# Optimization experiments

Hardware: AMD Instinct MI355X
Metric: run time of the kernel (lower is better)

Reference implementation:

```python
import jax, jax.numpy as jnp
import numpy as np

B, L, S, D, H, NS, NSLOT = 2, 2048, 2048, 1024, 16, 8, 512
HD = D // H


def _silu(x):
    return x * jax.nn.sigmoid(x)


def _layernorm(x, g, b, eps=1e-5):
    mu = jnp.mean(x, axis=-1, keepdims=True)
    var = jnp.var(x, axis=-1, keepdims=True)
    return (x - mu) * jax.lax.rsqrt(var + eps) * g + b


def setup_inputs() -> dict:
    key = jax.random.key(0)
    ks = jax.random.split(key, 12)
    x_q = jax.random.normal(ks[0], (B, L, D), dtype=jnp.float32)
    x_idx = jax.random.randint(ks[1], (B, S), 0, NSLOT)
    E_slots = jax.random.normal(ks[2], (NSLOT, D), dtype=jnp.float32)
    # EMA decay rates close to 1 so multi-scale gates stay non-degenerate over S steps
    rhos = 1.0 - 0.005 * jax.random.uniform(ks[3], (NS,), dtype=jnp.float32)
    C_seq = jax.random.uniform(ks[4], (B, L, NS), dtype=jnp.float32)
    s = 1.0 / np.sqrt(D)
    Wq = jax.random.normal(ks[5], (D, D), dtype=jnp.float32) * s
    Wk = jax.random.normal(ks[6], (D, D), dtype=jnp.float32) * s
    Wv = jax.random.normal(ks[7], (D, D), dtype=jnp.float32) * s
    Wo = jax.random.normal(ks[8], (D, D), dtype=jnp.float32) * s
    Wpe = jax.random.normal(ks[9], (D, NS), dtype=jnp.float32) * (1.0 / np.sqrt(NS))
    ln_kv_g = jnp.ones((D,), jnp.float32); ln_kv_b = jnp.zeros((D,), jnp.float32)
    ln_q_g = jnp.ones((D,), jnp.float32); ln_q_b = jnp.zeros((D,), jnp.float32)
    return dict(x_q=x_q, x_idx=x_idx, E_slots=E_slots, rhos=rhos, C_seq=C_seq,
                Wq=Wq, Wk=Wk, Wv=Wv, Wo=Wo, Wpe=Wpe,
                ln_kv_g=ln_kv_g, ln_kv_b=ln_kv_b, ln_q_g=ln_q_g, ln_q_b=ln_q_b)


def reference(x_q, x_idx, E_slots, rhos, C_seq, Wq, Wk, Wv, Wo, Wpe,
              ln_kv_g, ln_kv_b, ln_q_g, ln_q_b):
    # --- KV side: memory = ln_kv(E_slots); K/V = proj(memory); gather by slot id ---
    mem = _layernorm(E_slots, ln_kv_g, ln_kv_b)          # [NSLOT, D]
    Ek = mem @ Wk.T                                       # [NSLOT, D]
    Ev = mem @ Wv.T
    K = Ek[x_idx]                                         # [B, S, D] embedding lookup
    V = Ev[x_idx]
    # --- multiplicative EMA gate per kv position: c[s,m] = rho_m^(age) ---
    ages = (S - 1 - jnp.arange(S)).astype(x_q.dtype)      # [S]
    c_kv = jnp.power(rhos[None, :], ages[:, None])        # [S, NS]
    gate_kv = _silu(c_kv @ Wpe.T)                         # [S, D] = SiLU(pe_proj(C))
    K = K * gate_kv[None]
    V = V * gate_kv[None]
    # --- symmetric query gating: Q = q_proj(ln_q(x_q * SiLU(pe_proj(C_seq)))) ---
    gate_q = _silu(C_seq @ Wpe.T)                         # [B, L, D]
    Q = _layernorm(x_q * gate_q, ln_q_g, ln_q_b) @ Wq.T   # [B, L, D]
    # --- multi-head softmax attention ---
    q = Q.reshape(B, L, H, HD)
    k = K.reshape(B, S, H, HD)
    v = V.reshape(B, S, H, HD)
    scores = jnp.einsum('blhd,bshd->bhls', q, k) / np.sqrt(HD).astype(np.float32)
    attn = jax.nn.softmax(scores, axis=-1)                # [B, H, L, S]
    out = jnp.einsum('bhls,bshd->blhd', attn, v).reshape(B, L, D)
    return out @ Wo.T                                     # o_proj (dropout = identity, eval)
```

## Files before the change

kernel.cpp:

```cpp
#include <hip/hip_runtime.h>
#include <cmath>
#include <cstddef>

namespace {

constexpr int cB = 2, cL = 2048, cS = 2048, cD = 1024, cH = 16, cNS = 8, cNSLOT = 512, cHD = 64;

typedef __attribute__((ext_vector_type(8))) short short8;
typedef __attribute__((ext_vector_type(4))) float f32x4;

#define MFMA16(a, b, c) __builtin_amdgcn_mfma_f32_16x16x32_bf16((a), (b), (c), 0, 0, 0)

__device__ __forceinline__ float sigmoidf_(float x) { return 1.f / (1.f + __expf(-x)); }

__device__ __forceinline__ unsigned short f2bf(float x) {
  union { float f; unsigned u; } c; c.f = x;
  unsigned r = c.u + 0x7FFFu + ((c.u >> 16) & 1u);
  return (unsigned short)(r >> 16);
}
__device__ __forceinline__ float bf2f(unsigned short h) {
  union { unsigned u; float f; } c; c.u = ((unsigned)h) << 16;
  return c.f;
}

__device__ __forceinline__ void async16(const void* g, void* l) {
  __builtin_amdgcn_global_load_lds((const __attribute__((address_space(1))) void*)g,
                                   (__attribute__((address_space(3))) void*)l, 16, 0, 0);
}

__global__ __launch_bounds__(256) void prep_all_kernel(
    const float* __restrict__ Wq, const float* __restrict__ Wk,
    const float* __restrict__ Wv, const float* __restrict__ Wo,
    unsigned short* __restrict__ Wqh, unsigned short* __restrict__ Wql,
    unsigned short* __restrict__ Wkh, unsigned short* __restrict__ Wkl,
    unsigned short* __restrict__ Wvh, unsigned short* __restrict__ Wvl,
    unsigned short* __restrict__ Woh, unsigned short* __restrict__ Wol,
    const float* __restrict__ E, const float* __restrict__ lnkv_g,
    const float* __restrict__ lnkv_b, unsigned short* __restrict__ mh,
    const float* __restrict__ rhos,
    const float* __restrict__ Wpe, float* __restrict__ gkv,
    const float* __restrict__ xq, const float* __restrict__ Cseq,
    const float* __restrict__ lnq_g, const float* __restrict__ lnq_b,
    unsigned short* __restrict__ Yh) {
  __shared__ float sC[cNS];
  __shared__ float rbuf[8];
  const int bid = blockIdx.x;
  const int tid = threadIdx.x;

  if (bid < 2048) {
    const int wid = bid >> 9;
    const size_t off = ((size_t)(bid & 511) * 256 + tid) * 8;
    const float* src = wid == 0 ? Wq : wid == 1 ? Wk : wid == 2 ? Wv : Wo;
    unsigned short* dh = wid == 0 ? Wqh : wid == 1 ? Wkh : wid == 2 ? Wvh : Woh;
    unsigned short* dl = wid == 0 ? Wql : wid == 1 ? Wkl : wid == 2 ? Wvl : Wol;
    const float4 a = *(const float4*)(src + off);
    const float4 b = *(const float4*)(src + off + 4);
    float v[8] = {a.x, a.y, a.z, a.w, b.x, b.y, b.z, b.w};
    unsigned short h8[8], l8[8];
#pragma unroll
    for (int j = 0; j < 8; j++) {
      h8[j] = f2bf(v[j]);
      l8[j] = f2bf(v[j] - bf2f(h8[j]));
    }
    *(uint4*)(dh + off) = *(uint4*)h8;
    *(uint4*)(dl + off) = *(uint4*)l8;
  } else if (bid < 2560) {
    const int row = bid - 2048;
    const int d0 = tid * 4;
    const float4 x = *(const float4*)(E + (size_t)row * cD + d0);
    float s1 = x.x + x.y + x.z + x.w;
    float s2 = x.x * x.x + x.y * x.y + x.z * x.z + x.w * x.w;
#pragma unroll
    for (int o = 32; o > 0; o >>= 1) { s1 += __shfl_xor(s1, o, 64); s2 += __shfl_xor(s2, o, 64); }
    if ((tid & 63) == 0) { rbuf[tid >> 6] = s1; rbuf[4 + (tid >> 6)] = s2; }
    __syncthreads();
    s1 = rbuf[0] + rbuf[1] + rbuf[2] + rbuf[3];
    s2 = rbuf[4] + rbuf[5] + rbuf[6] + rbuf[7];
    const float mean = s1 * (1.f / cD);
    const float var = s2 * (1.f / cD) - mean * mean;
    const float inv = rsqrtf(var + 1e-5f);
    const float4 g = *(const float4*)(lnkv_g + d0);
    const float4 b = *(const float4*)(lnkv_b + d0);
    unsigned short h4[4];
    h4[0] = f2bf((x.x - mean) * inv * g.x + b.x);
    h4[1] = f2bf((x.y - mean) * inv * g.y + b.y);
    h4[2] = f2bf((x.z - mean) * inv * g.z + b.z);
    h4[3] = f2bf((x.w - mean) * inv * g.w + b.w);
    *(uint2*)(mh + (size_t)row * cD + d0) = *(uint2*)h4;
  } else if (bid < 4608) {
    const int s = bid - 2560;
    if (tid < cNS) {
      const float age = (float)(cS - 1 - s);
      sC[tid] = __expf(age * __logf(rhos[tid]));
    }
    __syncthreads();
    const int d0 = tid * 4;
    float4 o4;
#pragma unroll
    for (int j = 0; j < 4; j++) {
      const float* wr = Wpe + (size_t)(d0 + j) * cNS;
      float gs = 0.f;
#pragma unroll
      for (int m = 0; m < cNS; m++) gs += sC[m] * wr[m];
      ((float*)&o4)[j] = gs * sigmoidf_(gs);
    }
    *(float4*)(gkv + (size_t)s * cD + d0) = o4;
  } else {
    const int row = bid - 4608;
    if (tid < cNS) sC[tid] = Cseq[(size_t)row * cNS + tid];
    __syncthreads();
    const int d0 = tid * 4;
    const float4 x = *(const float4*)(xq + (size_t)row * cD + d0);
    float y[4];
    float s1 = 0.f, s2 = 0.f;
#pragma unroll
    for (int j = 0; j < 4; j++) {
      const float* wr = Wpe + (size_t)(d0 + j) * cNS;
      float gs = 0.f;
#pragma unroll
      for (int m = 0; m < cNS; m++) gs += sC[m] * wr[m];
      const float val = ((const float*)&x)[j] * gs * sigmoidf_(gs);
      y[j] = val;
      s1 += val;
      s2 += val * val;
    }
#pragma unroll
    for (int o = 32; o > 0; o >>= 1) { s1 += __shfl_xor(s1, o, 64); s2 += __shfl_xor(s2, o, 64); }
    if ((tid & 63) == 0) { rbuf[tid >> 6] = s1; rbuf[4 + (tid >> 6)] = s2; }
    __syncthreads();
    s1 = rbuf[0] + rbuf[1] + rbuf[2] + rbuf[3];
    s2 = rbuf[4] + rbuf[5] + rbuf[6] + rbuf[7];
    const float mean = s1 * (1.f / cD);
    const float var = s2 * (1.f / cD) - mean * mean;
    const float inv = rsqrtf(var + 1e-5f);
    const float4 g = *(const float4*)(lnq_g + d0);
    const float4 b = *(const float4*)(lnq_b + d0);
    unsigned short h4[4];
    h4[0] = f2bf((y[0] - mean) * inv * g.x + b.x);
    h4[1] = f2bf((y[1] - mean) * inv * g.y + b.y);
    h4[2] = f2bf((y[2] - mean) * inv * g.z + b.z);
    h4[3] = f2bf((y[3] - mean) * inv * g.w + b.w);
    *(uint2*)(Yh + (size_t)row * cD + d0) = *(uint2*)h4;
  }
}

template <int MODE>
__global__ __launch_bounds__(256, 2) void gemm2_kernel(
    const unsigned short* __restrict__ Ahi,
    const unsigned short* __restrict__ Whi0, const unsigned short* __restrict__ Wlo0,
    const unsigned short* __restrict__ Whi1, const unsigned short* __restrict__ Wlo1,
    float* __restrict__ Cf0, float* __restrict__ Cf1,
    unsigned short* __restrict__ Chi,
    int M, int N, int K, float scale) {
  __shared__ __align__(16) unsigned short sA[2][128 * 32];
  __shared__ __align__(16) unsigned short sBh[2][64 * 32];
  __shared__ __align__(16) unsigned short sBl[2][64 * 32];
  const unsigned short* Whi = blockIdx.z ? Whi1 : Whi0;
  const unsigned short* Wlo = blockIdx.z ? Wlo1 : Wlo0;
  float* Cf = blockIdx.z ? Cf1 : Cf0;
  const int tid = threadIdx.x;
  const int wave = tid >> 6, lane = tid & 63;
  const int quad = lane >> 4, l16 = lane & 15;
  const int m0 = blockIdx.y * 128, n0 = blockIdx.x * 64;
  const int wy = wave >> 1, wx = wave & 1;
  const int sg = (lane & 3) ^ ((lane >> 3) & 3);
  const int srow = lane >> 2;

  f32x4 acc[4][2];
#pragma unroll
  for (int i = 0; i < 4; i++)
#pragma unroll
    for (int j = 0; j < 2; j++) acc[i][j] = (f32x4){0.f, 0.f, 0.f, 0.f};

  auto stage = [&](int buf, int k0) {
#pragma unroll
    for (int c = 0; c < 2; c++) {
      const int row = c * 64 + wave * 16 + srow;
      const size_t ga = (size_t)(m0 + row) * K + k0 + sg * 8;
      async16(Ahi + ga, &sA[buf][(c * 64 + wave * 16) * 32]);
    }
    const int rowb = wave * 16 + srow;
    const size_t gb = (size_t)(n0 + rowb) * K + k0 + sg * 8;
    async16(Whi + gb, &sBh[buf][wave * 16 * 32]);
    async16(Wlo + gb, &sBl[buf][wave * 16 * 32]);
  };

  stage(0, 0);
  __syncthreads();
  const int aswz = (l16 >> 1) & 3;
  int buf = 0;
  for (int k0 = 0; k0 < K; k0 += 32, buf ^= 1) {
    if (k0 + 32 < K) stage(buf ^ 1, k0 + 32);
    short8 bh[2], bl2[2];
#pragma unroll
    for (int tj = 0; tj < 2; tj++) {
      const int br = (wx * 32 + tj * 16 + l16) * 32 + ((quad ^ aswz) * 8);
      bh[tj] = *(const short8*)&sBh[buf][br];
      bl2[tj] = *(const short8*)&sBl[buf][br];
    }
#pragma unroll
    for (int ti = 0; ti < 4; ti++) {
      const int ar = (wy * 64 + ti * 16 + l16) * 32 + ((quad ^ aswz) * 8);
      const short8 ah = *(const short8*)&sA[buf][ar];
#pragma unroll
      for (int tj = 0; tj < 2; tj++) {
        acc[ti][tj] = MFMA16(ah, bh[tj], acc[ti][tj]);
        acc[ti][tj] = MFMA16(ah, bl2[tj], acc[ti][tj]);
      }
    }
    __syncthreads();
  }

#pragma unroll
  for (int ti = 0; ti < 4; ti++)
#pragma unroll
    for (int tj = 0; tj < 2; tj++) {
      const int row = m0 + wy * 64 + ti * 16 + quad * 4;
      const int col = n0 + wx * 32 + tj * 16 + l16;
#pragma unroll
      for (int r = 0; r < 4; r++) {
        const size_t idx = (size_t)(row + r) * N + col;
        if constexpr (MODE == 0) {
          Cf[idx] = acc[ti][tj][r];
        } else {
          Chi[idx] = f2bf(acc[ti][tj][r] * scale);
        }
      }
    }
}

__global__ __launch_bounds__(256) void prep_kv_kernel(
    const float* __restrict__ Ek, const float* __restrict__ Ev,
    const float* __restrict__ gkv, const int* __restrict__ xidx,
    unsigned short* __restrict__ Khi, unsigned short* __restrict__ Vthi) {
  __shared__ float tile[64][65];
  const int bid = blockIdx.x;
  const int tid = threadIdx.x;
  if (bid < 2048) {
    const int t = bid * 256 + tid;
    const int d0 = (t & 127) * 8;
    const int s = (t >> 7) & (cS - 1);
    const int b = t >> 18;
    const int slot = xidx[b * cS + s];
    const float4 e0 = *(const float4*)(Ek + (size_t)slot * cD + d0);
    const float4 e1 = *(const float4*)(Ek + (size_t)slot * cD + d0 + 4);
    const float4 g0 = *(const float4*)(gkv + (size_t)s * cD + d0);
    const float4 g1 = *(const float4*)(gkv + (size_t)s * cD + d0 + 4);
    float v[8] = {e0.x * g0.x, e0.y * g0.y, e0.z * g0.z, e0.w * g0.w,
                  e1.x * g1.x, e1.y * g1.y, e1.z * g1.z, e1.w * g1.w};
    unsigned short h8[8];
#pragma unroll
    for (int j = 0; j < 8; j++) h8[j] = f2bf(v[j]);
    *(uint4*)(Khi + (size_t)(b * cS + s) * cD + d0) = *(uint4*)h8;
  } else {
    const int local = bid - 2048;
    const int s0 = (local & 31) * 64;
    const int d0 = ((local >> 5) & 15) * 64;
    const int b = local >> 9;
    const int sl = tid >> 4;
    const int dl = (tid & 15) * 4;
#pragma unroll
    for (int it = 0; it < 4; it++) {
      const int s = s0 + sl + it * 16;
      const int slot = xidx[b * cS + s];
      const float4 e = *(const float4*)(Ev + (size_t)slot * cD + d0 + dl);
      const float4 g = *(const float4*)(gkv + (size_t)s * cD + d0 + dl);
      tile[sl + it * 16][dl + 0] = e.x * g.x;
      tile[sl + it * 16][dl + 1] = e.y * g.y;
      tile[sl + it * 16][dl + 2] = e.z * g.z;
      tile[sl + it * 16][dl + 3] = e.w * g.w;
    }
    __syncthreads();
    const int dr = tid >> 3;
    const int sc = (tid & 7) * 8;
#pragma unroll
    for (int it = 0; it < 2; it++) {
      const int d = d0 + dr + it * 32;
      unsigned short h8[8];
#pragma unroll
      for (int j = 0; j < 8; j++) h8[j] = f2bf(tile[sc + j][dr + it * 32]);
      *(uint4*)(Vthi + (size_t)(b * cD + d) * cS + s0 + sc) = *(uint4*)h8;
    }
  }
}

__global__ __launch_bounds__(256, 2) void attn_mfma_kernel(
    const unsigned short* __restrict__ qhi,
    const unsigned short* __restrict__ Khi,
    const unsigned short* __restrict__ Vthi,
    unsigned short* __restrict__ AOhi) {
  __shared__ __align__(16) unsigned short sKh[64 * 64];
  __shared__ __align__(16) unsigned short sVh[64 * 64];
  __shared__ __align__(16) unsigned short sP[4][2][16][76];

  const int tid = threadIdx.x;
  const int wave = tid >> 6, lane = tid & 63;
  const int quad = lane >> 4, l16 = lane & 15;
  const int lB = blockIdx.x * 128;
  const int h = blockIdx.y, b = blockIdx.z;

  short8 qh[2][2];
#pragma unroll
  for (int t = 0; t < 2; t++) {
    const size_t base =
        (size_t)(b * cL + lB + wave * 32 + t * 16 + l16) * cD + h * cHD + quad * 8;
    qh[t][0] = *(const short8*)(qhi + base);
    qh[t][1] = *(const short8*)(qhi + base + 32);
  }

  short8 ones;
#pragma unroll
  for (int i = 0; i < 8; i++) ones[i] = (short)0x3F80;

  f32x4 O[2][4], dacc[2];
#pragma unroll
  for (int t = 0; t < 2; t++) {
#pragma unroll
    for (int i = 0; i < 4; i++) O[t][i] = (f32x4){0.f, 0.f, 0.f, 0.f};
    dacc[t] = (f32x4){0.f, 0.f, 0.f, 0.f};
  }

  const int srow8 = lane >> 3;
  const int sg = (lane & 7) ^ srow8;

  const int r0 = (wave * 2 + 0) * 8 + srow8;
  const int r1 = (wave * 2 + 1) * 8 + srow8;
  const size_t kb0 = (size_t)(b * cS + r0) * cD + h * cHD + sg * 8;
  const size_t kb1 = (size_t)(b * cS + r1) * cD + h * cHD + sg * 8;
  const size_t vb0 = (size_t)(b * cD + h * cHD + r0) * cS + sg * 8;
  const size_t vb1 = (size_t)(b * cD + h * cHD + r1) * cS + sg * 8;

  uint4 k0h, v0h, k1h, v1h;
  k0h = *(const uint4*)(Khi + kb0);
  v0h = *(const uint4*)(Vthi + vb0);
  k1h = *(const uint4*)(Khi + kb1);
  v1h = *(const uint4*)(Vthi + vb1);

  const int j0 = wave * 2, j1 = wave * 2 + 1;

  for (int s0 = 0; s0 < cS; s0 += 64) {
    __syncthreads();
    *(uint4*)&sKh[j0 * 512 + lane * 8] = k0h;
    *(uint4*)&sVh[j0 * 512 + lane * 8] = v0h;
    *(uint4*)&sKh[j1 * 512 + lane * 8] = k1h;
    *(uint4*)&sVh[j1 * 512 + lane * 8] = v1h;
    __syncthreads();

    {
      const int sn = (s0 + 64) & (cS - 1);
      const size_t kc = (size_t)sn * cD;
      k0h = *(const uint4*)(Khi + kb0 + kc);
      v0h = *(const uint4*)(Vthi + vb0 + sn);
      k1h = *(const uint4*)(Khi + kb1 + kc);
      v1h = *(const uint4*)(Vthi + vb1 + sn);
    }

    f32x4 sc[2][4];
#pragma unroll
    for (int t = 0; t < 2; t++)
#pragma unroll
      for (int st = 0; st < 4; st++) sc[t][st] = (f32x4){0.f, 0.f, 0.f, 0.f};
#pragma unroll
    for (int st = 0; st < 4; st++) {
      const int srw = st * 16 + l16;
#pragma unroll
      for (int ks = 0; ks < 2; ks++) {
        const int slot = (ks * 4 + quad) ^ (srw & 7);
        const short8 kfh = *(const short8*)&sKh[srw * 64 + slot * 8];
        sc[0][st] = MFMA16(qh[0][ks], kfh, sc[0][st]);
        sc[1][st] = MFMA16(qh[1][ks], kfh, sc[1][st]);
      }
    }

#pragma unroll
    for (int t = 0; t < 2; t++)
#pragma unroll
      for (int st = 0; st < 4; st++)
#pragma unroll
        for (int r = 0; r < 4; r++)
          sP[wave][t][quad * 4 + r][st * 16 + l16] =
              f2bf(__builtin_amdgcn_exp2f(sc[t][st][r]));

    short8 pfh[2][2];
#pragma unroll
    for (int t = 0; t < 2; t++) {
      pfh[t][0] = *(const short8*)&sP[wave][t][l16][quad * 8];
      pfh[t][1] = *(const short8*)&sP[wave][t][l16][32 + quad * 8];
    }

#pragma unroll
    for (int dt = 0; dt < 4; dt++) {
      const int drw = dt * 16 + l16;
#pragma unroll
      for (int ss = 0; ss < 2; ss++) {
        const int slot = (ss * 4 + quad) ^ (drw & 7);
        const short8 vfh = *(const short8*)&sVh[drw * 64 + slot * 8];
        O[0][dt] = MFMA16(pfh[0][ss], vfh, O[0][dt]);
        O[1][dt] = MFMA16(pfh[1][ss], vfh, O[1][dt]);
      }
    }
#pragma unroll
    for (int t = 0; t < 2; t++) {
      dacc[t] = MFMA16(pfh[t][0], ones, dacc[t]);
      dacc[t] = MFMA16(pfh[t][1], ones, dacc[t]);
    }
  }

#pragma unroll
  for (int t = 0; t < 2; t++) {
    float inv[4];
#pragma unroll
    for (int r = 0; r < 4; r++) inv[r] = 1.f / dacc[t][r];
#pragma unroll
    for (int dt = 0; dt < 4; dt++)
#pragma unroll
      for (int r = 0; r < 4; r++) {
        const size_t l = (size_t)(b * cL + lB + wave * 32 + t * 16 + quad * 4 + r);
        AOhi[l * cD + h * cHD + dt * 16 + l16] = f2bf(O[t][dt][r] * inv[r]);
      }
  }
}

}

extern "C" void kernel_launch(void* const* d_in, const int* in_sizes, int n_in,
                              void* d_out, int out_size, void* d_ws, size_t ws_size,
                              hipStream_t stream) {
  (void)in_sizes; (void)n_in; (void)out_size; (void)ws_size;
  const float* x_q = (const float*)d_in[0];
  const int* x_idx = (const int*)d_in[1];
  const float* E_slots = (const float*)d_in[2];
  const float* rhos = (const float*)d_in[3];
  const float* C_seq = (const float*)d_in[4];
  const float* Wq = (const float*)d_in[5];
  const float* Wk = (const float*)d_in[6];
  const float* Wv = (const float*)d_in[7];
  const float* Wo = (const float*)d_in[8];
  const float* Wpe = (const float*)d_in[9];
  const float* ln_kv_g = (const float*)d_in[10];
  const float* ln_kv_b = (const float*)d_in[11];
  const float* ln_q_g = (const float*)d_in[12];
  const float* ln_q_b = (const float*)d_in[13];
  float* out = (float*)d_out;

  float* ws = (float*)d_ws;
  unsigned short* memhi = (unsigned short*)(ws + 0);
  unsigned short* Wkhi = (unsigned short*)(ws + 262144);
  unsigned short* Wklo = (unsigned short*)(ws + 786432);
  unsigned short* Wvhi = (unsigned short*)(ws + 1310720);
  unsigned short* Wvlo = (unsigned short*)(ws + 1835008);
  float* gkv = ws + 2359296;
  unsigned short* Wqhi = (unsigned short*)(ws + 4456448);
  unsigned short* Wqlo = (unsigned short*)(ws + 4980736);
  unsigned short* Wohi = (unsigned short*)(ws + 5505024);
  unsigned short* Wolo = (unsigned short*)(ws + 6029312);
  float* Ek = ws + 6553600;
  float* Ev = ws + 7077888;
  unsigned short* Yhi = (unsigned short*)(ws + 7602176);
  unsigned short* AOhi = (unsigned short*)(ws + 7602176);
  unsigned short* qhi = (unsigned short*)(ws + 9699328);
  unsigned short* Khi = (unsigned short*)(ws + 11796480);
  unsigned short* Vthi = (unsigned short*)(ws + 13893632);

  constexpr float kQScale = 0.125f * 1.44269504088896340736f;

  prep_all_kernel<<<8704, 256, 0, stream>>>(
      Wq, Wk, Wv, Wo, Wqhi, Wqlo, Wkhi, Wklo, Wvhi, Wvlo, Wohi, Wolo,
      E_slots, ln_kv_g, ln_kv_b, memhi, rhos, Wpe, gkv,
      x_q, C_seq, ln_q_g, ln_q_b, Yhi);
  gemm2_kernel<0><<<dim3(16, 4, 2), 256, 0, stream>>>(
      memhi, Wkhi, Wklo, Wvhi, Wvlo, Ek, Ev, nullptr, cNSLOT, cD, cD, 1.f);
  prep_kv_kernel<<<3072, 256, 0, stream>>>(Ek, Ev, gkv, x_idx, Khi, Vthi);
  gemm2_kernel<1><<<dim3(16, 32, 1), 256, 0, stream>>>(
      Yhi, Wqhi, Wqlo, Wqhi, Wqlo, nullptr, nullptr, qhi, cB * cL, cD, cD, kQScale);
  attn_mfma_kernel<<<dim3(cL / 128, cH, cB), 256, 0, stream>>>(qhi, Khi, Vthi, AOhi);
  gemm2_kernel<0><<<dim3(16, 32, 1), 256, 0, stream>>>(
      AOhi, Wohi, Wolo, Wohi, Wolo, out, out, nullptr, cB * cL, cD, cD, 1.f);
}
```

Baseline: 267.4 us.

## Merge K/V and Q projections into one launch, halve attention block size

The K/V slot projection GEMM and the Q projection GEMM now run in a single launch that splits work by block index, which removes a launch and lets the small K/V work overlap the Q GEMM. The attention kernel drops from 4 waves to 2 waves per block and covers 64 query rows per block, giving twice as many blocks. Each thread now loads 4 K/V rows, and the P tile is stored as packed bf16 pairs, then unpacked with perm instructions. Launch bounds are raised to 3 blocks per CU, trading register budget for occupancy.

```diff
diff --git a/kernel.cpp b/kernel.cpp
--- a/kernel.cpp
+++ b/kernel.cpp
@@ -21,6 +21,18 @@
 __device__ __forceinline__ float bf2f(unsigned short h) {
   union { unsigned u; float f; } c; c.u = ((unsigned)h) << 16;
   return c.f;
+}
+
+__device__ __forceinline__ void unpack8(const uint4 a, const uint4 b, short8& p0, short8& p1) {
+  const unsigned p[8] = {a.x, a.y, a.z, a.w, b.x, b.y, b.z, b.w};
+  union { unsigned u[4]; short8 s; } H, L;
+#pragma unroll
+  for (int i = 0; i < 4; i++) {
+    H.u[i] = __builtin_amdgcn_perm(p[2 * i + 1], p[2 * i], 0x05040100u);
+    L.u[i] = __builtin_amdgcn_perm(p[2 * i + 1], p[2 * i], 0x07060302u);
+  }
+  p0 = H.s;
+  p1 = L.s;
 }
 
 __device__ __forceinline__ void async16(const void* g, void* l) {
@@ -145,26 +157,19 @@
 }
 
 template <int MODE>
-__global__ __launch_bounds__(256, 2) void gemm2_kernel(
+__device__ __forceinline__ void gemm2_body(
     const unsigned short* __restrict__ Ahi,
-    const unsigned short* __restrict__ Whi0, const unsigned short* __restrict__ Wlo0,
-    const unsigned short* __restrict__ Whi1, const unsigned short* __restrict__ Wlo1,
-    float* __restrict__ Cf0, float* __restrict__ Cf1,
-    unsigned short* __restrict__ Chi,
-    int M, int N, int K, float scale) {
-  __shared__ __align__(16) unsigned short sA[2][128 * 32];
-  __shared__ __align__(16) unsigned short sBh[2][64 * 32];
-  __shared__ __align__(16) unsigned short sBl[2][64 * 32];
-  const unsigned short* Whi = blockIdx.z ? Whi1 : Whi0;
-  const unsigned short* Wlo = blockIdx.z ? Wlo1 : Wlo0;
-  float* Cf = blockIdx.z ? Cf1 : Cf0;
+    const unsigned short* __restrict__ Whi, const unsigned short* __restrict__ Wlo,
+    float* __restrict__ Cf, unsigned short* __restrict__ Chi,
+    int m0, int n0, int N, int K, float scale,
+    unsigned short* sA, unsigned short* sBh, unsigned short* sBl) {
   const int tid = threadIdx.x;
   const int wave = tid >> 6, lane = tid & 63;
   const int quad = lane >> 4, l16 = lane & 15;
-  const int m0 = blockIdx.y * 128, n0 = blockIdx.x * 64;
   const int wy = wave >> 1, wx = wave & 1;
   const int sg = (lane & 3) ^ ((lane >> 3) & 3);
   const int srow = lane >> 2;
+  (void)srow;
 
   f32x4 acc[4][2];
 #pragma unroll
@@ -175,14 +180,14 @@
   auto stage = [&](int buf, int k0) {
 #pragma unroll
     for (int c = 0; c < 2; c++) {
-      const int row = c * 64 + wave * 16 + srow;
+      const int row = c * 64 + wave * 16 + (lane >> 2);
       const size_t ga = (size_t)(m0 + row) * K + k0 + sg * 8;
-      async16(Ahi + ga, &sA[buf][(c * 64 + wave * 16) * 32]);
-    }
-    const int rowb = wave * 16 + srow;
+      async16(Ahi + ga, sA + buf * 4096 + (c * 64 + wave * 16) * 32);
+    }
+    const int rowb = wave * 16 + (lane >> 2);
     const size_t gb = (size_t)(n0 + rowb) * K + k0 + sg * 8;
-    async16(Whi + gb, &sBh[buf][wave * 16 * 32]);
-    async16(Wlo + gb, &sBl[buf][wave * 16 * 32]);
+    async16(Whi + gb, sBh + buf * 2048 + wave * 16 * 32);
+    async16(Wlo + gb, sBl + buf * 2048 + wave * 16 * 32);
   };
 
   stage(0, 0);
@@ -195,13 +200,13 @@
 #pragma unroll
     for (int tj = 0; tj < 2; tj++) {
       const int br = (wx * 32 + tj * 16 + l16) * 32 + ((quad ^ aswz) * 8);
-      bh[tj] = *(const short8*)&sBh[buf][br];
-      bl2[tj] = *(const short8*)&sBl[buf][br];
+      bh[tj] = *(const short8*)(sBh + buf * 2048 + br);
+      bl2[tj] = *(const short8*)(sBl + buf * 2048 + br);
     }
 #pragma unroll
     for (int ti = 0; ti < 4; ti++) {
       const int ar = (wy * 64 + ti * 16 + l16) * 32 + ((quad ^ aswz) * 8);
-      const short8 ah = *(const short8*)&sA[buf][ar];
+      const short8 ah = *(const short8*)(sA + buf * 4096 + ar);
 #pragma unroll
       for (int tj = 0; tj < 2; tj++) {
         acc[ti][tj] = MFMA16(ah, bh[tj], acc[ti][tj]);
@@ -227,6 +232,41 @@
         }
       }
     }
+}
+
+__global__ __launch_bounds__(256, 3) void gemm_qkv_kernel(
+    const unsigned short* __restrict__ memhi,
+    const unsigned short* __restrict__ Wkhi, const unsigned short* __restrict__ Wklo,
+    const unsigned short* __restrict__ Wvhi, const unsigned short* __restrict__ Wvlo,
+    float* __restrict__ Ek, float* __restrict__ Ev,
+    const unsigned short* __restrict__ Yhi,
+    const unsigned short* __restrict__ Wqhi, const unsigned short* __restrict__ Wqlo,
+    unsigned short* __restrict__ qhi, float qscale) {
+  __shared__ __align__(16) unsigned short sA[2 * 128 * 32];
+  __shared__ __align__(16) unsigned short sBh[2 * 64 * 32];
+  __shared__ __align__(16) unsigned short sBl[2 * 64 * 32];
+  const int bid = blockIdx.x;
+  if (bid < 128) {
+    const int z = bid >> 6, rem = bid & 63;
+    const int m0 = (rem >> 4) * 128, n0 = (rem & 15) * 64;
+    gemm2_body<0>(memhi, z ? Wvhi : Wkhi, z ? Wvlo : Wklo, z ? Ev : Ek, nullptr,
+                  m0, n0, cD, cD, 1.f, sA, sBh, sBl);
+  } else {
+    const int lid = bid - 128;
+    const int m0 = (lid >> 4) * 128, n0 = (lid & 15) * 64;
+    gemm2_body<1>(Yhi, Wqhi, Wqlo, nullptr, qhi, m0, n0, cD, cD, qscale, sA, sBh, sBl);
+  }
+}
+
+__global__ __launch_bounds__(256, 3) void gemm_o_kernel(
+    const unsigned short* __restrict__ AOhi,
+    const unsigned short* __restrict__ Wohi, const unsigned short* __restrict__ Wolo,
+    float* __restrict__ out) {
+  __shared__ __align__(16) unsigned short sA[2 * 128 * 32];
+  __shared__ __align__(16) unsigned short sBh[2 * 64 * 32];
+  __shared__ __align__(16) unsigned short sBl[2 * 64 * 32];
+  gemm2_body<0>(AOhi, Wohi, Wolo, out, nullptr, blockIdx.y * 128, blockIdx.x * 64,
+                cD, cD, 1.f, sA, sBh, sBl);
 }
 
 __global__ __launch_bounds__(256) void prep_kv_kernel(
@@ -284,19 +324,19 @@
   }
 }
 
-__global__ __launch_bounds__(256, 2) void attn_mfma_kernel(
+__global__ __launch_bounds__(128, 3) void attn_mfma_kernel(
     const unsigned short* __restrict__ qhi,
     const unsigned short* __restrict__ Khi,
     const unsigned short* __restrict__ Vthi,
     unsigned short* __restrict__ AOhi) {
   __shared__ __align__(16) unsigned short sKh[64 * 64];
   __shared__ __align__(16) unsigned short sVh[64 * 64];
-  __shared__ __align__(16) unsigned short sP[4][2][16][76];
+  __shared__ __align__(16) unsigned int sP32[2][16][68];
 
   const int tid = threadIdx.x;
   const int wave = tid >> 6, lane = tid & 63;
   const int quad = lane >> 4, l16 = lane & 15;
-  const int lB = blockIdx.x * 128;
+  const int lB = blockIdx.x * 64;
   const int h = blockIdx.y, b = blockIdx.z;
 
   short8 qh[2][2];
@@ -323,36 +363,54 @@
   const int srow8 = lane >> 3;
   const int sg = (lane & 7) ^ srow8;
 
-  const int r0 = (wave * 2 + 0) * 8 + srow8;
-  const int r1 = (wave * 2 + 1) * 8 + srow8;
+  const int r0 = (wave * 4 + 0) * 8 + srow8;
+  const int r1 = (wave * 4 + 1) * 8 + srow8;
+  const int r2 = (wave * 4 + 2) * 8 + srow8;
+  const int r3 = (wave * 4 + 3) * 8 + srow8;
   const size_t kb0 = (size_t)(b * cS + r0) * cD + h * cHD + sg * 8;
   const size_t kb1 = (size_t)(b * cS + r1) * cD + h * cHD + sg * 8;
+  const size_t kb2 = (size_t)(b * cS + r2) * cD + h * cHD + sg * 8;
+  const size_t kb3 = (size_t)(b * cS + r3) * cD + h * cHD + sg * 8;
   const size_t vb0 = (size_t)(b * cD + h * cHD + r0) * cS + sg * 8;
   const size_t vb1 = (size_t)(b * cD + h * cHD + r1) * cS + sg * 8;
-
-  uint4 k0h, v0h, k1h, v1h;
-  k0h = *(const uint4*)(Khi + kb0);
-  v0h = *(const uint4*)(Vthi + vb0);
-  k1h = *(const uint4*)(Khi + kb1);
-  v1h = *(const uint4*)(Vthi + vb1);
-
-  const int j0 = wave * 2, j1 = wave * 2 + 1;
+  const size_t vb2 = (size_t)(b * cD + h * cHD + r2) * cS + sg * 8;
+  const size_t vb3 = (size_t)(b * cD + h * cHD + r3) * cS + sg * 8;
+
+  uint4 k0, k1, k2, k3, v0, v1, v2, v3;
+  k0 = *(const uint4*)(Khi + kb0);
+  k1 = *(const uint4*)(Khi + kb1);
+  k2 = *(const uint4*)(Khi + kb2);
+  k3 = *(const uint4*)(Khi + kb3);
+  v0 = *(const uint4*)(Vthi + vb0);
+  v1 = *(const uint4*)(Vthi + vb1);
+  v2 = *(const uint4*)(Vthi + vb2);
+  v3 = *(const uint4*)(Vthi + vb3);
+
+  const int j0 = wave * 4;
 
   for (int s0 = 0; s0 < cS; s0 += 64) {
     __syncthreads();
-    *(uint4*)&sKh[j0 * 512 + lane * 8] = k0h;
-    *(uint4*)&sVh[j0 * 512 + lane * 8] = v0h;
-    *(uint4*)&sKh[j1 * 512 + lane * 8] = k1h;
-    *(uint4*)&sVh[j1 * 512 + lane * 8] = v1h;
+    *(uint4*)&sKh[(j0 + 0) * 512 + lane * 8] = k0;
+    *(uint4*)&sKh[(j0 + 1) * 512 + lane * 8] = k1;
+    *(uint4*)&sKh[(j0 + 2) * 512 + lane * 8] = k2;
+    *(uint4*)&sKh[(j0 + 3) * 512 + lane * 8] = k3;
+    *(uint4*)&sVh[(j0 + 0) * 512 + lane * 8] = v0;
+    *(uint4*)&sVh[(j0 + 1) * 512 + lane * 8] = v1;
+    *(uint4*)&sVh[(j0 + 2) * 512 + lane * 8] = v2;
+    *(uint4*)&sVh[(j0 + 3) * 512 + lane * 8] = v3;
     __syncthreads();
 
     {
       const int sn = (s0 + 64) & (cS - 1);
       const size_t kc = (size_t)sn * cD;
-      k0h = *(const uint4*)(Khi + kb0 + kc);
-      v0h = *(const uint4*)(Vthi + vb0 + sn);
-      k1h = *(const uint4*)(Khi + kb1 + kc);
-      v1h = *(const uint4*)(Vthi + vb1 + sn);
+      k0 = *(const uint4*)(Khi + kb0 + kc);
+      k1 = *(const uint4*)(Khi + kb1 + kc);
+      k2 = *(const uint4*)(Khi + kb2 + kc);
+      k3 = *(const uint4*)(Khi + kb3 + kc);
+      v0 = *(const uint4*)(Vthi + vb0 + sn);
+      v1 = *(const uint4*)(Vthi + vb1 + sn);
+      v2 = *(const uint4*)(Vthi + vb2 + sn);
+      v3 = *(const uint4*)(Vthi + vb3 + sn);
     }
 
     f32x4 sc[2][4];
@@ -373,19 +431,20 @@
     }
 
 #pragma unroll
-    for (int t = 0; t < 2; t++)
-#pragma unroll
-      for (int st = 0; st < 4; st++)
-#pragma unroll
-        for (int r = 0; r < 4; r++)
-          sP[wave][t][quad * 4 + r][st * 16 + l16] =
-              f2bf(__builtin_amdgcn_exp2f(sc[t][st][r]));
-
-    short8 pfh[2][2];
-#pragma unroll
-    for (int t = 0; t < 2; t++) {
-      pfh[t][0] = *(const short8*)&sP[wave][t][l16][quad * 8];
-      pfh[t][1] = *(const short8*)&sP[wave][t][l16][32 + quad * 8];
+    for (int st = 0; st < 4; st++)
+#pragma unroll
+      for (int r = 0; r < 4; r++) {
+        const unsigned u0 = f2bf(__builtin_amdgcn_exp2f(sc[0][st][r]));
+        const unsigned u1 = f2bf(__builtin_amdgcn_exp2f(sc[1][st][r]));
+        sP32[wave][quad * 4 + r][st * 16 + l16] = (u1 << 16) | u0;
+      }
+
+    short8 pf0[2], pf1[2];
+#pragma unroll
+    for (int ss = 0; ss < 2; ss++) {
+      const uint4 pa = *(const uint4*)&sP32[wave][l16][ss * 32 + quad * 8];
+      const uint4 pb = *(const uint4*)&sP32[wave][l16][ss * 32 + quad * 8 + 4];
+      unpack8(pa, pb, pf0[ss], pf1[ss]);
     }
 
 #pragma unroll
@@ -395,15 +454,14 @@
       for (int ss = 0; ss < 2; ss++) {
         const int slot = (ss * 4 + quad) ^ (drw & 7);
         const short8 vfh = *(const short8*)&sVh[drw * 64 + slot * 8];
-        O[0][dt] = MFMA16(pfh[0][ss], vfh, O[0][dt]);
-        O[1][dt] = MFMA16(pfh[1][ss], vfh, O[1][dt]);
+        O[0][dt] = MFMA16(pf0[ss], vfh, O[0][dt]);
+        O[1][dt] = MFMA16(pf1[ss], vfh, O[1][dt]);
       }
     }
-#pragma unroll
-    for (int t = 0; t < 2; t++) {
-      dacc[t] = MFMA16(pfh[t][0], ones, dacc[t]);
-      dacc[t] = MFMA16(pfh[t][1], ones, dacc[t]);
-    }
+    dacc[0] = MFMA16(pf0[0], ones, dacc[0]);
+    dacc[0] = MFMA16(pf0[1], ones, dacc[0]);
+    dacc[1] = MFMA16(pf1[0], ones, dacc[1]);
+    dacc[1] = MFMA16(pf1[1], ones, dacc[1]);
   }
 
 #pragma unroll
@@ -468,12 +526,9 @@
       Wq, Wk, Wv, Wo, Wqhi, Wqlo, Wkhi, Wklo, Wvhi, Wvlo, Wohi, Wolo,
       E_slots, ln_kv_g, ln_kv_b, memhi, rhos, Wpe, gkv,
       x_q, C_seq, ln_q_g, ln_q_b, Yhi);
-  gemm2_kernel<0><<<dim3(16, 4, 2), 256, 0, stream>>>(
-      memhi, Wkhi, Wklo, Wvhi, Wvlo, Ek, Ev, nullptr, cNSLOT, cD, cD, 1.f);
+  gemm_qkv_kernel<<<640, 256, 0, stream>>>(
+      memhi, Wkhi, Wklo, Wvhi, Wvlo, Ek, Ev, Yhi, Wqhi, Wqlo, qhi, kQScale);
   prep_kv_kernel<<<3072, 256, 0, stream>>>(Ek, Ev, gkv, x_idx, Khi, Vthi);
-  gemm2_kernel<1><<<dim3(16, 32, 1), 256, 0, stream>>>(
-      Yhi, Wqhi, Wqlo, Wqhi, Wqlo, nullptr, nullptr, qhi, cB * cL, cD, cD, kQScale);
-  attn_mfma_kernel<<<dim3(cL / 128, cH, cB), 256, 0, stream>>>(qhi, Khi, Vthi, AOhi);
-  gemm2_kernel<0><<<dim3(16, 32, 1), 256, 0, stream>>>(
-      AOhi, Wohi, Wolo, Wohi, Wolo, out, out, nullptr, cB * cL, cD, cD, 1.f);
-}
+  attn_mfma_kernel<<<dim3(cL / 64, cH, cB), 128, 0, stream>>>(qhi, Khi, Vthi, AOhi);
+  gemm_o_kernel<<<dim3(16, 32), 256, 0, stream>>>(AOhi, Wohi, Wolo, out);
+}
```

After: 261.5 us. 1.02x faster.
